# Kernel optimization log

Hardware: AMD Instinct MI355X
Metric: run time of the kernel (lower is better)

## Reference

```python
import jax, jax.numpy as jnp
import numpy as np

NUM_FILLERS = 50257
NUM_ROLES = 512
FILLER_DIM = 256  # D1
ROLE_DIM = 256    # D2
OUT_DIM = 1024
B, S = 64, 128


def setup_inputs() -> dict:
    key = jax.random.key(0)
    k1, k2, k3, k4, k5, k6 = jax.random.split(key, 6)
    fillers = jax.random.randint(k1, (B, S), 0, NUM_FILLERS)
    roles = jax.random.randint(k2, (B, S), 0, NUM_ROLES)
    filler_table = jax.random.normal(k3, (NUM_FILLERS, FILLER_DIM), dtype=jnp.float32)
    role_table = jax.random.normal(k4, (NUM_ROLES, ROLE_DIM), dtype=jnp.float32)
    # nn.Linear(filler_dim*role_dim, final_layer_width)
    lim = 1.0 / np.sqrt(FILLER_DIM * ROLE_DIM)
    W = jax.random.uniform(k5, (OUT_DIM, FILLER_DIM * ROLE_DIM), minval=-lim, maxval=lim, dtype=jnp.float32)
    b = jax.random.uniform(k6, (OUT_DIM,), minval=-lim, maxval=lim, dtype=jnp.float32)
    return {"fillers": fillers, "roles": roles, "filler_table": filler_table,
            "role_table": role_table, "W": W, "b": b}


def reference(fillers, roles, filler_table, role_table, W, b):
    # Embedding lookups: [B, S, D1] and [B, S, D2]
    f = filler_table[fillers]
    r = role_table[roles]
    # Sum over S of flattened outer products f_s (x) r_s -> [B, D1, D2]
    # (equivalent to the original's S*B rank-1 bmm + sum over S, fused as one GEMM)
    tp = jnp.einsum('bsd,bse->bde', f, r)
    tp = tp.reshape(f.shape[0], FILLER_DIM * ROLE_DIM)  # [B, D1*D2]
    # Final linear layer
    return tp @ W.T + b
```

## Files before the change

### kernel.cpp

```cpp
#include <hip/hip_runtime.h>
#include <hip/hip_bf16.h>

#define B_DIM 64
#define S_DIM 128
#define D1    256
#define D2    256
#define KTOT  65536
#define NOUT  1024

#define KSPLIT 64
#define KCHUNK (KTOT / KSPLIT)
#define BK     128
#define BKITERS (KCHUNK / BK)
#define KSTEPS  (BK / 32)
#define WPAD   16

typedef __attribute__((ext_vector_type(8))) short bf16x8;
typedef __attribute__((ext_vector_type(4))) float f32x4;

__device__ inline unsigned pack2bf16(float lo, float hi) {
    unsigned ulo = __float_as_uint(lo);
    unsigned uhi = __float_as_uint(hi);
    ulo = (ulo + 0x8000u) >> 16;
    uhi = (uhi + 0x8000u) & 0xffff0000u;
    return ulo | uhi;
}

__global__ __launch_bounds__(256) void tp_kernel(const int* __restrict__ fillers,
                                                 const int* __restrict__ roles,
                                                 const float* __restrict__ ftab,
                                                 const float* __restrict__ rtab,
                                                 unsigned short* __restrict__ tp) {
    const int b     = blockIdx.x;
    const int dbase = blockIdx.y * 32;
    __shared__ float f_sh[S_DIM][32];
    __shared__ int   ridx[S_DIM];
    const int t = threadIdx.x;

    const int* fb = fillers + b * S_DIM;
    for (int i = t; i < S_DIM * 32; i += 256) {
        int s = i >> 5, dl = i & 31;
        f_sh[s][dl] = ftab[(long)fb[s] * D1 + dbase + dl];
    }
    if (t < S_DIM) ridx[t] = roles[b * S_DIM + t];
    __syncthreads();

    const int dsub = t >> 6;
    const int et   = t & 63;
    float acc[8][4];
#pragma unroll
    for (int i = 0; i < 8; ++i)
#pragma unroll
        for (int j = 0; j < 4; ++j) acc[i][j] = 0.f;

    for (int s = 0; s < S_DIM; ++s) {
        const float4 rv = *(const float4*)(rtab + ridx[s] * D2 + et * 4);
        const float4 f0 = *(const float4*)&f_sh[s][dsub * 8];
        const float4 f1 = *(const float4*)&f_sh[s][dsub * 8 + 4];
        float fv[8] = {f0.x, f0.y, f0.z, f0.w, f1.x, f1.y, f1.z, f1.w};
        float rr[4] = {rv.x, rv.y, rv.z, rv.w};
#pragma unroll
        for (int dl = 0; dl < 8; ++dl)
#pragma unroll
            for (int c = 0; c < 4; ++c) acc[dl][c] += fv[dl] * rr[c];
    }

    unsigned short* dst = tp + (size_t)b * KTOT + (size_t)(dbase + dsub * 8) * D2 + et * 4;
#pragma unroll
    for (int dl = 0; dl < 8; ++dl) {
        uint2 pp;
        pp.x = pack2bf16(acc[dl][0], acc[dl][1]);
        pp.y = pack2bf16(acc[dl][2], acc[dl][3]);
        *(uint2*)(dst + (size_t)dl * D2) = pp;
    }
}

__global__ __launch_bounds__(256, 4) void gemm_kernel(const unsigned short* __restrict__ tp,
                                                      const float* __restrict__ W,
                                                      float* __restrict__ part) {
    const int nt  = blockIdx.x;
    const int ks  = blockIdx.y;
    const int w   = threadIdx.x >> 6;
    const int L   = threadIdx.x & 63;
    const int l16 = L & 15;
    const int lq  = L >> 4;
    const int t   = threadIdx.x;
    const int ncol  = nt * 64 + w * 16;
    const int kbase = ks * KCHUNK;

    __shared__ unsigned short wlds[64][BK + WPAD];

    const int srow = t >> 5;
    const int sc4  = t & 31;
    const float* wsrc = W + (size_t)(nt * 64 + srow) * KTOT + kbase + sc4 * 4;

    const unsigned short* tpp = tp + (size_t)l16 * KTOT + kbase + lq * 8;

    f32x4 acc[4];
#pragma unroll
    for (int mt = 0; mt < 4; ++mt) acc[mt] = (f32x4){0.f, 0.f, 0.f, 0.f};

    float4 wreg[8];
#pragma unroll
    for (int i = 0; i < 8; ++i)
        wreg[i] = *(const float4*)(wsrc + (size_t)(8 * i) * KTOT);

    for (int bk = 0; bk < BKITERS; ++bk) {
#pragma unroll
        for (int i = 0; i < 8; ++i) {
            uint2 pp;
            pp.x = pack2bf16(wreg[i].x, wreg[i].y);
            pp.y = pack2bf16(wreg[i].z, wreg[i].w);
            *(uint2*)&wlds[srow + 8 * i][sc4 * 4] = pp;
        }
        __syncthreads();

        if (bk + 1 < BKITERS) {
            const float* wn = wsrc + (bk + 1) * BK;
#pragma unroll
            for (int i = 0; i < 8; ++i)
                wreg[i] = *(const float4*)(wn + (size_t)(8 * i) * KTOT);
        }

#pragma unroll
        for (int kk = 0; kk < KSTEPS; ++kk) {
            const int koff = bk * BK + kk * 32;
            bf16x8 a0 = *(const bf16x8*)(tpp + koff);
            bf16x8 a1 = *(const bf16x8*)(tpp + koff + 16 * KTOT);
            bf16x8 a2 = *(const bf16x8*)(tpp + koff + 32 * KTOT);
            bf16x8 a3 = *(const bf16x8*)(tpp + koff + 48 * KTOT);
            bf16x8 bw = *(const bf16x8*)&wlds[w * 16 + l16][kk * 32 + lq * 8];
            acc[0] = __builtin_amdgcn_mfma_f32_16x16x32_bf16(a0, bw, acc[0], 0, 0, 0);
            acc[1] = __builtin_amdgcn_mfma_f32_16x16x32_bf16(a1, bw, acc[1], 0, 0, 0);
            acc[2] = __builtin_amdgcn_mfma_f32_16x16x32_bf16(a2, bw, acc[2], 0, 0, 0);
            acc[3] = __builtin_amdgcn_mfma_f32_16x16x32_bf16(a3, bw, acc[3], 0, 0, 0);
        }
        __syncthreads();
    }

    float* pp = part + (size_t)ks * (B_DIM * NOUT) + ncol + l16;
#pragma unroll
    for (int mt = 0; mt < 4; ++mt)
#pragma unroll
        for (int r = 0; r < 4; ++r)
            pp[(size_t)(mt * 16 + lq * 4 + r) * NOUT] = acc[mt][r];
}

__global__ __launch_bounds__(256) void reduce_kernel(const float* __restrict__ part,
                                                     const float* __restrict__ bias,
                                                     float* __restrict__ out) {
    const int i    = blockIdx.x * 256 + threadIdx.x;
    const size_t o = (size_t)i * 4;
    const float* p = part + o;
    f32x4 a0 = {0.f, 0.f, 0.f, 0.f};
    f32x4 a1 = {0.f, 0.f, 0.f, 0.f};
#pragma unroll 8
    for (int ks = 0; ks < KSPLIT; ks += 2) {
        f32x4 x = *(const f32x4*)(p + (size_t)ks * (B_DIM * NOUT));
        f32x4 y = *(const f32x4*)(p + (size_t)(ks + 1) * (B_DIM * NOUT));
        a0 += x;
        a1 += y;
    }
    f32x4 bv = *(const f32x4*)(bias + (o & (NOUT - 1)));
    f32x4 r  = a0 + a1 + bv;
    *(f32x4*)(out + o) = r;
}

extern "C" void kernel_launch(void* const* d_in, const int* in_sizes, int n_in,
                              void* d_out, int out_size, void* d_ws, size_t ws_size,
                              hipStream_t stream) {
    const int*   fillers = (const int*)d_in[0];
    const int*   roles   = (const int*)d_in[1];
    const float* ftab    = (const float*)d_in[2];
    const float* rtab    = (const float*)d_in[3];
    const float* W       = (const float*)d_in[4];
    const float* bias    = (const float*)d_in[5];
    float* out = (float*)d_out;

    float*          part = (float*)d_ws;
    unsigned short* tp   = (unsigned short*)((char*)d_ws + (size_t)KSPLIT * B_DIM * NOUT * 4);

    hipLaunchKernelGGL(tp_kernel, dim3(B_DIM, 8), dim3(256), 0, stream,
                       fillers, roles, ftab, rtab, tp);
    hipLaunchKernelGGL(gemm_kernel, dim3(16, KSPLIT), dim3(256), 0, stream, tp, W, part);
    hipLaunchKernelGGL(reduce_kernel, dim3(64), dim3(256), 0, stream, part, bias, out);
}
```

Baseline: 447.3 us.

## Retile GEMM to 16-column N tiles with atomic split-K, drop reduce kernel

The GEMM now uses 64 N-tiles of 16 columns by 16 K-slices instead of 16 N-tiles of 64 columns by 64 K-slices. Each wave owns 16 batch rows instead of one wave per N sub-tile covering all 64 rows. Partial sums go straight into the output with float atomicAdd, and tp_kernel first writes the bias into the output, so the partial-sum workspace and the reduce kernel are gone. This removes a large partial buffer write and read plus one launch. The cost is more atomics, non-deterministic summation order, and each block loading fewer W rows, which changes the reuse of tp against W.

```diff
diff --git a/kernel.cpp b/kernel.cpp
--- a/kernel.cpp
+++ b/kernel.cpp
@@ -1,5 +1,4 @@
 #include <hip/hip_runtime.h>
-#include <hip/hip_bf16.h>
 
 #define B_DIM 64
 #define S_DIM 128
@@ -8,12 +7,14 @@
 #define KTOT  65536
 #define NOUT  1024
 
-#define KSPLIT 64
-#define KCHUNK (KTOT / KSPLIT)
-#define BK     128
-#define BKITERS (KCHUNK / BK)
+#define NTILE   16
+#define NTILES  (NOUT / NTILE)
+#define KSLICES 16
+#define KC      (KTOT / KSLICES)
+#define BK      128
+#define CHUNKS  (KC / BK)
 #define KSTEPS  (BK / 32)
-#define WPAD   16
+#define WPAD    8
 
 typedef __attribute__((ext_vector_type(8))) short bf16x8;
 typedef __attribute__((ext_vector_type(4))) float f32x4;
@@ -30,12 +31,20 @@
                                                  const int* __restrict__ roles,
                                                  const float* __restrict__ ftab,
                                                  const float* __restrict__ rtab,
-                                                 unsigned short* __restrict__ tp) {
+                                                 unsigned short* __restrict__ tp,
+                                                 const float* __restrict__ bias,
+                                                 float* __restrict__ out) {
     const int b     = blockIdx.x;
     const int dbase = blockIdx.y * 32;
     __shared__ float f_sh[S_DIM][32];
     __shared__ int   ridx[S_DIM];
     const int t = threadIdx.x;
+
+    if (blockIdx.y == 0) {
+        const int i = blockIdx.x * 256 + t;
+        f32x4 bv = *(const f32x4*)(bias + ((i * 4) & (NOUT - 1)));
+        *(f32x4*)(out + (size_t)i * 4) = bv;
+    }
 
     const int* fb = fillers + b * S_DIM;
     for (int i = t; i < S_DIM * 32; i += 256) {
@@ -77,93 +86,58 @@
 
 __global__ __launch_bounds__(256, 4) void gemm_kernel(const unsigned short* __restrict__ tp,
                                                       const float* __restrict__ W,
-                                                      float* __restrict__ part) {
-    const int nt  = blockIdx.x;
-    const int ks  = blockIdx.y;
-    const int w   = threadIdx.x >> 6;
-    const int L   = threadIdx.x & 63;
+                                                      float* __restrict__ out) {
+    const int n0    = blockIdx.x * NTILE;
+    const int kbase = blockIdx.y * KC;
+    const int t   = threadIdx.x;
+    const int w   = t >> 6;
+    const int L   = t & 63;
     const int l16 = L & 15;
     const int lq  = L >> 4;
-    const int t   = threadIdx.x;
-    const int ncol  = nt * 64 + w * 16;
-    const int kbase = ks * KCHUNK;
 
-    __shared__ unsigned short wlds[64][BK + WPAD];
+    __shared__ unsigned short wlds[NTILE][BK + WPAD];
 
-    const int srow = t >> 5;
-    const int sc4  = t & 31;
-    const float* wsrc = W + (size_t)(nt * 64 + srow) * KTOT + kbase + sc4 * 4;
+    const int srow = t >> 4;
+    const int sc4  = t & 15;
+    const float* wsrc = W + (size_t)(n0 + srow) * KTOT + kbase + sc4 * 4;
 
-    const unsigned short* tpp = tp + (size_t)l16 * KTOT + kbase + lq * 8;
+    const unsigned short* tpp = tp + (size_t)(w * 16 + l16) * KTOT + kbase + lq * 8;
 
-    f32x4 acc[4];
-#pragma unroll
-    for (int mt = 0; mt < 4; ++mt) acc[mt] = (f32x4){0.f, 0.f, 0.f, 0.f};
+    f32x4 acc = {0.f, 0.f, 0.f, 0.f};
 
-    float4 wreg[8];
-#pragma unroll
-    for (int i = 0; i < 8; ++i)
-        wreg[i] = *(const float4*)(wsrc + (size_t)(8 * i) * KTOT);
+    float4 wr0 = *(const float4*)(wsrc);
+    float4 wr1 = *(const float4*)(wsrc + 64);
 
-    for (int bk = 0; bk < BKITERS; ++bk) {
-#pragma unroll
-        for (int i = 0; i < 8; ++i) {
-            uint2 pp;
-            pp.x = pack2bf16(wreg[i].x, wreg[i].y);
-            pp.y = pack2bf16(wreg[i].z, wreg[i].w);
-            *(uint2*)&wlds[srow + 8 * i][sc4 * 4] = pp;
-        }
+    for (int bk = 0; bk < CHUNKS; ++bk) {
+        uint2 p0, p1;
+        p0.x = pack2bf16(wr0.x, wr0.y);
+        p0.y = pack2bf16(wr0.z, wr0.w);
+        p1.x = pack2bf16(wr1.x, wr1.y);
+        p1.y = pack2bf16(wr1.z, wr1.w);
+        *(uint2*)&wlds[srow][sc4 * 4]      = p0;
+        *(uint2*)&wlds[srow][sc4 * 4 + 64] = p1;
         __syncthreads();
 
-        if (bk + 1 < BKITERS) {
-            const float* wn = wsrc + (bk + 1) * BK;
-#pragma unroll
-            for (int i = 0; i < 8; ++i)
-                wreg[i] = *(const float4*)(wn + (size_t)(8 * i) * KTOT);
+        if (bk + 1 < CHUNKS) {
+            const float* wn = wsrc + (size_t)(bk + 1) * BK;
+            wr0 = *(const float4*)(wn);
+            wr1 = *(const float4*)(wn + 64);
         }
 
 #pragma unroll
         for (int kk = 0; kk < KSTEPS; ++kk) {
-            const int koff = bk * BK + kk * 32;
-            bf16x8 a0 = *(const bf16x8*)(tpp + koff);
-            bf16x8 a1 = *(const bf16x8*)(tpp + koff + 16 * KTOT);
-            bf16x8 a2 = *(const bf16x8*)(tpp + koff + 32 * KTOT);
-            bf16x8 a3 = *(const bf16x8*)(tpp + koff + 48 * KTOT);
-            bf16x8 bw = *(const bf16x8*)&wlds[w * 16 + l16][kk * 32 + lq * 8];
-            acc[0] = __builtin_amdgcn_mfma_f32_16x16x32_bf16(a0, bw, acc[0], 0, 0, 0);
-            acc[1] = __builtin_amdgcn_mfma_f32_16x16x32_bf16(a1, bw, acc[1], 0, 0, 0);
-            acc[2] = __builtin_amdgcn_mfma_f32_16x16x32_bf16(a2, bw, acc[2], 0, 0, 0);
-            acc[3] = __builtin_amdgcn_mfma_f32_16x16x32_bf16(a3, bw, acc[3], 0, 0, 0);
+            bf16x8 a = *(const bf16x8*)(tpp + bk * BK + kk * 32);
+            bf16x8 b = *(const bf16x8*)&wlds[l16][kk * 32 + lq * 8];
+            acc = __builtin_amdgcn_mfma_f32_16x16x32_bf16(a, b, acc, 0, 0, 0);
         }
         __syncthreads();
     }
 
-    float* pp = part + (size_t)ks * (B_DIM * NOUT) + ncol + l16;
+    const int m = w * 16 + lq * 4;
+    float* op = out + (size_t)m * NOUT + n0 + l16;
 #pragma unroll
-    for (int mt = 0; mt < 4; ++mt)
-#pragma unroll
-        for (int r = 0; r < 4; ++r)
-            pp[(size_t)(mt * 16 + lq * 4 + r) * NOUT] = acc[mt][r];
-}
-
-__global__ __launch_bounds__(256) void reduce_kernel(const float* __restrict__ part,
-                                                     const float* __restrict__ bias,
-                                                     float* __restrict__ out) {
-    const int i    = blockIdx.x * 256 + threadIdx.x;
-    const size_t o = (size_t)i * 4;
-    const float* p = part + o;
-    f32x4 a0 = {0.f, 0.f, 0.f, 0.f};
-    f32x4 a1 = {0.f, 0.f, 0.f, 0.f};
-#pragma unroll 8
-    for (int ks = 0; ks < KSPLIT; ks += 2) {
-        f32x4 x = *(const f32x4*)(p + (size_t)ks * (B_DIM * NOUT));
-        f32x4 y = *(const f32x4*)(p + (size_t)(ks + 1) * (B_DIM * NOUT));
-        a0 += x;
-        a1 += y;
-    }
-    f32x4 bv = *(const f32x4*)(bias + (o & (NOUT - 1)));
-    f32x4 r  = a0 + a1 + bv;
-    *(f32x4*)(out + o) = r;
+    for (int r = 0; r < 4; ++r)
+        atomicAdd(op + (size_t)r * NOUT, acc[r]);
 }
 
 extern "C" void kernel_launch(void* const* d_in, const int* in_sizes, int n_in,
@@ -177,11 +151,10 @@
     const float* bias    = (const float*)d_in[5];
     float* out = (float*)d_out;
 
-    float*          part = (float*)d_ws;
-    unsigned short* tp   = (unsigned short*)((char*)d_ws + (size_t)KSPLIT * B_DIM * NOUT * 4);
+    unsigned short* tp = (unsigned short*)d_ws;
 
     hipLaunchKernelGGL(tp_kernel, dim3(B_DIM, 8), dim3(256), 0, stream,
-                       fillers, roles, ftab, rtab, tp);
-    hipLaunchKernelGGL(gemm_kernel, dim3(16, KSPLIT), dim3(256), 0, stream, tp, W, part);
-    hipLaunchKernelGGL(reduce_kernel, dim3(64), dim3(256), 0, stream, part, bias, out);
+                       fillers, roles, ftab, rtab, tp, bias, out);
+    hipLaunchKernelGGL(gemm_kernel, dim3(NTILES, KSLICES), dim3(256), 0, stream,
+                       tp, W, out);
 }
```

Result: faster. 432.7 us (-3.3%).
